# Kernel optimization log

Measured on AMD Instinct MI355X. Metric: run time of the kernel, lower is better.

Reference implementation:

```python
import jax, jax.numpy as jnp
import numpy as np

DIM = 1024
HEADS = 16
DIM_HEAD = 64
INNER = HEADS * DIM_HEAD
B, N = 2, 2048


def rope_encoding(seq_len, dim_head):
    inv_freq = 1.0 / (10000.0 ** (jnp.arange(0, dim_head, 2, dtype=jnp.float32) / dim_head))
    pos = jnp.arange(seq_len, dtype=jnp.float32)
    sinusoid = pos[:, None] * inv_freq[None, :]          # [n, d/2]
    return jnp.concatenate([jnp.sin(sinusoid), jnp.cos(sinusoid)], axis=-1)  # [n, d]


def setup_inputs() -> dict:
    key = jax.random.key(0)
    k1, k2, k3, k4 = jax.random.split(key, 4)
    feats = jax.random.normal(k1, (B, N, DIM), dtype=jnp.float32)
    mask = jnp.ones((B, N), dtype=bool)
    # params (torch Linear: y = x @ W.T + b; store as [in, out] for x @ W)
    W_qkv = jax.random.normal(k2, (DIM, 3 * INNER), dtype=jnp.float32) / np.sqrt(DIM)
    W_out = jax.random.normal(k3, (INNER, DIM), dtype=jnp.float32) / np.sqrt(INNER)
    b_out = jax.random.normal(k4, (DIM,), dtype=jnp.float32) * 0.01
    return {"feats": feats, "W_qkv": W_qkv, "W_out": W_out, "b_out": b_out, "mask": mask}


def reference(feats, W_qkv, W_out, b_out, mask):
    b, n, _ = feats.shape
    h, d = HEADS, DIM_HEAD
    scale = d ** -0.5

    qkv = feats @ W_qkv                                   # [b, n, 3*inner]
    q, k, v = jnp.split(qkv, 3, axis=-1)
    to_bhnd = lambda t: t.reshape(b, n, h, d).transpose(0, 2, 1, 3)
    q, k, v = to_bhnd(q), to_bhnd(k), to_bhnd(v)          # [b, h, n, d]

    rope = rope_encoding(n, d)                            # [n, d]
    q = q + rope
    k = k + rope

    m = mask[:, None, :, None]                            # [b, 1, n, 1]
    neg_max = -jnp.finfo(k.dtype).max
    k = jnp.where(m, k, neg_max)

    q = jax.nn.softmax(q, axis=-1)                        # over feature dim
    k = jax.nn.softmax(k, axis=-2)                        # over sequence dim
    q = q * scale
    v = jnp.where(m, v, 0.0)

    context = jnp.einsum('bhnd,bhne->bhde', k, v)         # [b, h, d, d]
    out = jnp.einsum('bhde,bhnd->bhne', context, q)       # [b, h, n, d]
    out = out.transpose(0, 2, 1, 3).reshape(b, n, h * d)  # [b, n, inner]
    out = out @ W_out + b_out                             # [b, n, dim]

    attn = jnp.einsum('bhnd,bhmd->bhnm', q, k) * scale    # [b, h, n, n]
    return out, attn
```

## Files before the change

kernel.cpp:

```cpp
#include <hip/hip_runtime.h>
#include <cstddef>


#define BB     2
#define SEQ    2048
#define DIMM   1024
#define NHEADS 16
#define DH     64
#define TRIPLE 3072
#define ROWS   (BB*SEQ)
#define SCALE  0.125f

typedef unsigned short u16;
typedef unsigned int   u32;
typedef short s16x8 __attribute__((ext_vector_type(8)));
typedef float f32x4 __attribute__((ext_vector_type(4)));
typedef float vf4   __attribute__((ext_vector_type(4)));

static constexpr size_t WS_QB    = 0;
static constexpr size_t WS_KB    = 8388608;
static constexpr size_t WS_DEN   = 16777216;
static constexpr size_t WS_CTX   = 16785408;
static constexpr size_t WS_ROPET = 17309696;
static constexpr size_t WS_AQPK  = 17833984;
static constexpr size_t WS_W2PK  = 34611200;

static constexpr size_t SC_QKV  = 0;
static constexpr size_t SC_APK  = 50331648;
static constexpr size_t SC_WQPK = 67108864;

__device__ __forceinline__ u16 f2bf(float x) {
    u32 u = __float_as_uint(x);
    return (u16)((u + 0x7fffu + ((u >> 16) & 1u)) >> 16);
}
__device__ __forceinline__ float bf2f(u16 h) {
    return __uint_as_float(((u32)h) << 16);
}
__device__ __forceinline__ void glds16(const char* g, char* l) {
    __builtin_amdgcn_global_load_lds(
        (const __attribute__((address_space(1))) void*)g,
        (__attribute__((address_space(3))) void*)l, 16, 0, 0);
}

__device__ __forceinline__ void conv_pack_item(const float* __restrict__ src,
                                               u16* __restrict__ dst, int t)
{
    int g  = t & 3;
    int kb = (t >> 2) & 31;
    int row = t >> 7;
    const float* s = src + (size_t)row * 1024 + kb * 32 + 4 * g;
    float4 xa = *(const float4*)s;
    float4 xb = *(const float4*)(s + 16);
    float xs[8] = {xa.x, xa.y, xa.z, xa.w, xb.x, xb.y, xb.z, xb.w};
    s16x8 hv, lv;
    #pragma unroll
    for (int e = 0; e < 8; ++e) {
        u16 h = f2bf(xs[e]);
        hv[e] = (short)h;
        lv[e] = (short)f2bf(xs[e] - bf2f(h));
    }
    size_t rowc = (size_t)row * 256 + kb * 8;
    int sw = row & 7;
    *(s16x8*)(dst + (rowc + (size_t)(g ^ sw)) * 8)       = hv;
    *(s16x8*)(dst + (rowc + (size_t)((4 | g) ^ sw)) * 8) = lv;
}

__global__ __launch_bounds__(256)
void prologue(float4* __restrict__ denctx, float4* __restrict__ ropeT,
              const float* __restrict__ feats, u16* __restrict__ A_pk,
              const float* __restrict__ Wqkv, u16* __restrict__ Wq_pk)
{
    __shared__ float fb[32][128];
    const int bid = blockIdx.x, tid = threadIdx.x;
    if (bid < 130) {
        denctx[bid * 256 + tid] = float4{0.f, 0.f, 0.f, 0.f};
        return;
    }
    if (bid < 258) {
        int t = (bid - 130) * 256 + tid;
        int pos = t >> 4, r16 = t & 15;
        double a0 = (double)pos * pow(10000.0, -(double)r16 / 32.0);
        double a1 = (double)pos * pow(10000.0, -(double)(r16 + 16) / 32.0);
        float4 v;
        v.x = (float)sin(a0); v.y = (float)sin(a1);
        v.z = (float)cos(a0); v.w = (float)cos(a1);
        ropeT[t] = v;
        return;
    }
    if (bid < 2306) {
        conv_pack_item(feats, A_pk, (bid - 258) * 256 + tid);
        return;
    }
    {
        int cb = bid - 2306;
        int n0 = (cb % 24) * 128, kb = cb / 24, k0 = kb * 32;
        #pragma unroll
        for (int q = 0; q < 4; ++q) {
            int cc = q * 256 + tid;
            int kr = cc >> 5, nc = (cc & 31) * 4;
            *(float4*)&fb[kr][nc] = *(const float4*)&Wqkv[(size_t)(k0 + kr) * TRIPLE + n0 + nc];
        }
        __syncthreads();
        #pragma unroll
        for (int it = 0; it < 2; ++it) {
            int item = it * 256 + tid;
            int g = (item >> 7) & 3, n = item & 127;
            s16x8 hv, lv;
            #pragma unroll
            for (int e = 0; e < 4; ++e) {
                float x0 = fb[4 * g + e][n];
                float x1 = fb[16 + 4 * g + e][n];
                u16 h0 = f2bf(x0), h1 = f2bf(x1);
                hv[e]     = (short)h0;
                hv[e + 4] = (short)h1;
                lv[e]     = (short)f2bf(x0 - bf2f(h0));
                lv[e + 4] = (short)f2bf(x1 - bf2f(h1));
            }
            int row = n0 + n;
            size_t rowc = (size_t)row * 256 + kb * 8;
            int sw = row & 7;
            *(s16x8*)(Wq_pk + (rowc + (size_t)(g ^ sw)) * 8)       = hv;
            *(s16x8*)(Wq_pk + (rowc + (size_t)((4 | g) ^ sw)) * 8) = lv;
        }
    }
}

__global__ __launch_bounds__(256, 3)
void gemm_qkv(const u16* __restrict__ Ap, const u16* __restrict__ Bp,
              float* __restrict__ C, const float* __restrict__ ropeT,
              float* __restrict__ den)
{
    __shared__ __align__(16) char smem[32768];
    const int tid = threadIdx.x;
    const int lane = tid & 63, wid = tid >> 6;
    const int wi = wid >> 1, wj = wid & 1;
    const int r16 = lane & 15, g = lane >> 4;

    const int bid = blockIdx.x;
    const int swz = (bid & 7) * 96 + (bid >> 3);
    const int bx = swz % 24, by = swz / 24;
    const int brow = by * 128, bcol = bx * 128;

    const int srow = wid * 32 + (lane >> 3);
    const int sch  = lane & 7;
    const char* gA = (const char*)Ap + ((size_t)(brow + srow) * 256 + sch) * 16;
    const char* gB = (const char*)Bp + ((size_t)(bcol + srow) * 256 + sch) * 16;
    char* la = smem + wid * 4096;
    char* lb = smem + 16384 + wid * 4096;

    f32x4 acc[4][4] = {};
    size_t koff = 0;
    for (int kb = 0; kb < 32; ++kb, koff += 128) {
        #pragma unroll
        for (int q = 0; q < 4; ++q) {
            glds16(gA + (size_t)q * (8 * 4096) + koff, la + q * 1024);
            glds16(gB + (size_t)q * (8 * 4096) + koff, lb + q * 1024);
        }
        __syncthreads();
        s16x8 ah[4], al[4], bh[4], bl[4];
        #pragma unroll
        for (int i = 0; i < 4; ++i) {
            int ra = wi * 64 + i * 16 + r16;
            const s16x8* Ar = (const s16x8*)(smem + (size_t)ra * 128);
            ah[i] = Ar[g ^ (ra & 7)];
            al[i] = Ar[(4 | g) ^ (ra & 7)];
            int rb = wj * 64 + i * 16 + r16;
            const s16x8* Br = (const s16x8*)(smem + 16384 + (size_t)rb * 128);
            bh[i] = Br[g ^ (rb & 7)];
            bl[i] = Br[(4 | g) ^ (rb & 7)];
        }
        #pragma unroll
        for (int i = 0; i < 4; ++i)
            #pragma unroll
            for (int j = 0; j < 4; ++j) {
                acc[i][j] = __builtin_amdgcn_mfma_f32_16x16x32_bf16(ah[i], bh[j], acc[i][j], 0, 0, 0);
                acc[i][j] = __builtin_amdgcn_mfma_f32_16x16x32_bf16(ah[i], bl[j], acc[i][j], 0, 0, 0);
                acc[i][j] = __builtin_amdgcn_mfma_f32_16x16x32_bf16(al[i], bh[j], acc[i][j], 0, 0, 0);
            }
        __syncthreads();
    }

    const int pos0 = brow & (SEQ - 1);
    const vf4* rT = (const vf4*)ropeT;
    if (bx < 8) {
        #pragma unroll
        for (int i = 0; i < 4; ++i)
            #pragma unroll
            for (int r = 0; r < 4; ++r) {
                int rloc = wi * 64 + i * 16 + g * 4 + r;
                vf4 rv = rT[(size_t)(pos0 + rloc) * 16 + r16];
                float v[4];
                #pragma unroll
                for (int j = 0; j < 4; ++j) v[j] = acc[i][j][r] + rv[j];
                float m = fmaxf(fmaxf(v[0], v[1]), fmaxf(v[2], v[3]));
                #pragma unroll
                for (int o = 1; o <= 8; o <<= 1) m = fmaxf(m, __shfl_xor(m, o));
                float e[4];
                float s = 0.f;
                #pragma unroll
                for (int j = 0; j < 4; ++j) { e[j] = expf(v[j] - m); s += e[j]; }
                #pragma unroll
                for (int o = 1; o <= 8; o <<= 1) s += __shfl_xor(s, o);
                float inv = SCALE / s;
                size_t rb = (size_t)(brow + rloc) * TRIPLE + bcol + wj * 64;
                #pragma unroll
                for (int j = 0; j < 4; ++j)
                    C[rb + j * 16 + r16] = e[j] * inv;
            }
    } else if (bx < 16) {
        float dsum[4] = {0.f, 0.f, 0.f, 0.f};
        #pragma unroll
        for (int i = 0; i < 4; ++i)
            #pragma unroll
            for (int r = 0; r < 4; ++r) {
                int rloc = wi * 64 + i * 16 + g * 4 + r;
                vf4 rv = rT[(size_t)(pos0 + rloc) * 16 + r16];
                size_t rb = (size_t)(brow + rloc) * TRIPLE + bcol + wj * 64;
                #pragma unroll
                for (int j = 0; j < 4; ++j) {
                    float e = expf(acc[i][j][r] + rv[j]);
                    C[rb + j * 16 + r16] = e;
                    dsum[j] += e;
                }
            }
        const int bD = (brow >> 11) * DIMM;
        #pragma unroll
        for (int j = 0; j < 4; ++j) {
            float s = dsum[j];
            s += __shfl_xor(s, 16);
            s += __shfl_xor(s, 32);
            if (g == 0)
                atomicAdd(&den[bD + (bcol - DIMM) + wj * 64 + j * 16 + r16], s);
        }
    } else {
        #pragma unroll
        for (int i = 0; i < 4; ++i) {
            int row = brow + wi * 64 + i * 16 + g * 4;
            #pragma unroll
            for (int j = 0; j < 4; ++j) {
                int col = bcol + wj * 64 + j * 16 + r16;
                #pragma unroll
                for (int r = 0; r < 4; ++r)
                    C[(size_t)(row + r) * TRIPLE + col] = acc[i][j][r];
            }
        }
    }
}

__global__ __launch_bounds__(256)
void packctx(const float* __restrict__ qkv, const float* __restrict__ den,
             u16* __restrict__ qb, u16* __restrict__ kb,
             u16* __restrict__ Aq_pk, float* __restrict__ ctx)
{
    __shared__ float kt[32][64];
    __shared__ float vt[32][64];
    if (blockIdx.x < 2048) {
        int t = blockIdx.x * 256 + threadIdx.x;
        int g  = t & 3;
        int db = (t >> 2) & 1;
        int h  = (t >> 3) & 15;
        int row = t >> 7;
        int b = row >> 11, n = row & (SEQ - 1);
        size_t dst = ((size_t)(b * NHEADS + h) * SEQ + n) * 64 + db * 32 + g * 8;
        const float* sq = qkv + (size_t)row * TRIPLE + h * DH + db * 32 + 4 * g;
        {
            float4 xa = *(const float4*)sq;
            float4 xb = *(const float4*)(sq + 16);
            float xs[8] = {xa.x, xa.y, xa.z, xa.w, xb.x, xb.y, xb.z, xb.w};
            s16x8 hv, lv;
            #pragma unroll
            for (int e = 0; e < 8; ++e) {
                u16 hh = f2bf(xs[e]);
                hv[e] = (short)hh;
                lv[e] = (short)f2bf(xs[e] - bf2f(hh));
            }
            *(s16x8*)(qb + dst) = hv;
            int sw = row & 7;
            size_t base = (size_t)row * 2048 + (size_t)(h * 2 + db) * 64;
            *(s16x8*)(Aq_pk + base + (size_t)((g ^ sw) * 8))       = hv;
            *(s16x8*)(Aq_pk + base + (size_t)((((4 | g) ^ sw)) * 8)) = lv;
        }
        {
            const float* sk = sq + DIMM;
            const float* dn = den + (size_t)b * DIMM + h * DH + db * 32 + 4 * g;
            float4 xa = *(const float4*)sk;
            float4 xb = *(const float4*)(sk + 16);
            float4 da = *(const float4*)dn;
            float4 dc = *(const float4*)(dn + 16);
            float xs[8] = {xa.x / da.x, xa.y / da.y, xa.z / da.z, xa.w / da.w,
                           xb.x / dc.x, xb.y / dc.y, xb.z / dc.z, xb.w / dc.w};
            s16x8 hv;
            #pragma unroll
            for (int e = 0; e < 8; ++e) hv[e] = (short)f2bf(xs[e]);
            *(s16x8*)(kb + dst) = hv;
        }
        return;
    }
    int cb = blockIdx.x - 2048;
    int chunk = cb & 7, h = (cb >> 3) & 15, b = cb >> 7;
    int row0 = b * SEQ + chunk * 256;
    int d  = threadIdx.x & 63;
    int eg = threadIdx.x >> 6;
    float acc[16] = {};
    for (int t = 0; t < 8; ++t) {
        #pragma unroll
        for (int q = 0; q < 2; ++q) {
            int lf = threadIdx.x * 2 + q;
            int nn = lf >> 4;
            int c4 = (lf & 15) * 4;
            size_t base = (size_t)(row0 + t * 32 + nn) * TRIPLE + DIMM + h * DH + c4;
            *(float4*)&kt[nn][c4] = *(const float4*)&qkv[base];
            *(float4*)&vt[nn][c4] = *(const float4*)&qkv[base + DIMM];
        }
        __syncthreads();
        #pragma unroll 8
        for (int nn = 0; nn < 32; ++nn) {
            float kv = kt[nn][d];
            #pragma unroll
            for (int j = 0; j < 16; ++j)
                acc[j] = fmaf(kv, vt[nn][eg * 16 + j], acc[j]);
        }
        __syncthreads();
    }
    float rden = 1.f / den[(size_t)b * DIMM + h * DH + d];
    size_t cbase = ((size_t)(b * NHEADS + h)) * (DH * DH) + d * DH + eg * 16;
    #pragma unroll
    for (int j = 0; j < 16; ++j) atomicAdd(&ctx[cbase + j], acc[j] * rden);
}

__global__ __launch_bounds__(256)
void W2k(const float* __restrict__ ctx, const float* __restrict__ Wout,
         u16* __restrict__ W2_pk)
{
    __shared__ float cl[64][64];
    const int bid = blockIdx.x, tid = threadIdx.x;
    const int ct = bid & 7, h = (bid >> 3) & 15, b = bid >> 7;
    const float* C = ctx + ((size_t)(b * NHEADS + h)) * (DH * DH);
    for (int i = tid; i < DH * DH; i += 256) cl[i >> 6][i & 63] = C[i];
    __syncthreads();
    const int c = ct * 128 + (tid & 127);
    const int dg = tid >> 7;
    float acc[32] = {};
    for (int e = 0; e < 64; ++e) {
        float wv = Wout[(size_t)(h * 64 + e) * DIMM + c];
        #pragma unroll
        for (int r = 0; r < 32; ++r)
            acc[r] = fmaf(cl[dg * 32 + r][e], wv, acc[r]);
    }
    s16x8 hv[4], lv[4];
    #pragma unroll
    for (int r = 0; r < 32; ++r) {
        int g2 = (r & 15) >> 2;
        int elem = (r & 3) + 4 * (r >> 4);
        u16 hh = f2bf(acc[r]);
        hv[g2][elem] = (short)hh;
        lv[g2][elem] = (short)f2bf(acc[r] - bf2f(hh));
    }
    const int sw = c & 7;
    u16* base = W2_pk + (size_t)b * 2097152 + (size_t)c * 2048 + (size_t)(h * 2 + dg) * 64;
    #pragma unroll
    for (int g2 = 0; g2 < 4; ++g2) {
        *(s16x8*)(base + ((g2 ^ sw) * 8))       = hv[g2];
        *(s16x8*)(base + (((4 | g2) ^ sw) * 8)) = lv[g2];
    }
}

__global__ __launch_bounds__(256, 2)
void epilogue2(const u16* __restrict__ Aq_pk, const u16* __restrict__ W2_pk,
               float* __restrict__ outp, const float* __restrict__ bias,
               const u16* __restrict__ qb, const u16* __restrict__ kb,
               float* __restrict__ attn)
{
    __shared__ __align__(16) char smem[65536];
    const int tid = threadIdx.x;
    const int lane = tid & 63, wid = tid >> 6;
    const int r16 = lane & 15, g = lane >> 4;
    const int bid = blockIdx.x;

    if (bid % 17 == 0) {
        const int gb = bid / 17;
        const int wi = wid >> 1, wj = wid & 1;
        const int swz = (gb & 7) * 64 + (gb >> 3);
        const int bx = swz >> 6, by = swz & 63;
        const int brow = by * 64, bcol = bx * 128;
        const int srA = wid * 16 + (lane >> 3);
        const int srB = wid * 32 + (lane >> 3);
        const int sch = lane & 7;
        const char* gA = (const char*)Aq_pk + ((size_t)(brow + srA) * 256 + sch) * 16;
        const char* gB = (const char*)(W2_pk + (size_t)(brow >> 11) * 2097152)
                         + ((size_t)(bcol + srB) * 256 + sch) * 16;

        auto STAGE = [&](int buf, int kb2) {
            size_t koff = (size_t)kb2 * 128;
            char* a = smem + buf * 24576 + wid * 2048;
            char* b = smem + buf * 24576 + 8192 + wid * 4096;
            #pragma unroll
            for (int q = 0; q < 2; ++q)
                glds16(gA + (size_t)q * (8 * 4096) + koff, a + q * 1024);
            #pragma unroll
            for (int q = 0; q < 4; ++q)
                glds16(gB + (size_t)q * (8 * 4096) + koff, b + q * 1024);
        };

        f32x4 acc[2][4] = {};
        STAGE(0, 0);
        __syncthreads();
        for (int kb2 = 0; kb2 < 32; ++kb2) {
            const int cur = kb2 & 1;
            if (kb2 < 31) STAGE(cur ^ 1, kb2 + 1);
            const char* Ab = smem + cur * 24576;
            const char* Bb = smem + cur * 24576 + 8192;
            s16x8 ah[2], al[2], bh[4], bl[4];
            #pragma unroll
            for (int i = 0; i < 2; ++i) {
                int ra = wi * 32 + i * 16 + r16;
                const s16x8* Ar = (const s16x8*)(Ab + (size_t)ra * 128);
                ah[i] = Ar[g ^ (ra & 7)];
                al[i] = Ar[(4 | g) ^ (ra & 7)];
            }
            #pragma unroll
            for (int j = 0; j < 4; ++j) {
                int rb = wj * 64 + j * 16 + r16;
                const s16x8* Br = (const s16x8*)(Bb + (size_t)rb * 128);
                bh[j] = Br[g ^ (rb & 7)];
                bl[j] = Br[(4 | g) ^ (rb & 7)];
            }
            #pragma unroll
            for (int i = 0; i < 2; ++i)
                #pragma unroll
                for (int j = 0; j < 4; ++j) {
                    acc[i][j] = __builtin_amdgcn_mfma_f32_16x16x32_bf16(ah[i], bh[j], acc[i][j], 0, 0, 0);
                    acc[i][j] = __builtin_amdgcn_mfma_f32_16x16x32_bf16(ah[i], bl[j], acc[i][j], 0, 0, 0);
                    acc[i][j] = __builtin_amdgcn_mfma_f32_16x16x32_bf16(al[i], bh[j], acc[i][j], 0, 0, 0);
                }
            __syncthreads();
        }
        #pragma unroll
        for (int i = 0; i < 2; ++i) {
            int row = brow + wi * 32 + i * 16 + g * 4;
            #pragma unroll
            for (int j = 0; j < 4; ++j) {
                int col = bcol + wj * 64 + j * 16 + r16;
                float bv = bias[col];
                #pragma unroll
                for (int r = 0; r < 4; ++r)
                    outp[(size_t)(row + r) * DIMM + col] = acc[i][j][r] + bv;
            }
        }
        return;
    }

    const int ab = bid - bid / 17 - 1;
    const int bh = ab >> 8;
    const int n0 = ((ab >> 4) & 15) * 128, m0 = (ab & 15) * 128;
    const int wi = wid >> 1, wj = wid & 1;
    float* ost = (float*)smem;
    const u16* qB = qb + (size_t)bh * (SEQ * 64);
    const u16* kB = kb + (size_t)bh * (SEQ * 64);
    f32x4 acc[4][4] = {};
    #pragma unroll
    for (int db = 0; db < 2; ++db) {
        s16x8 a[4], b[4];
        #pragma unroll
        for (int i = 0; i < 4; ++i) {
            a[i] = *(const s16x8*)(qB + (size_t)(n0 + wi * 64 + i * 16 + r16) * 64 + db * 32 + g * 8);
            b[i] = *(const s16x8*)(kB + (size_t)(m0 + wj * 64 + i * 16 + r16) * 64 + db * 32 + g * 8);
        }
        #pragma unroll
        for (int i = 0; i < 4; ++i)
            #pragma unroll
            for (int j = 0; j < 4; ++j)
                acc[i][j] = __builtin_amdgcn_mfma_f32_16x16x32_bf16(a[i], b[j], acc[i][j], 0, 0, 0);
    }
    #pragma unroll
    for (int i = 0; i < 4; ++i)
        #pragma unroll
        for (int j = 0; j < 4; ++j)
            #pragma unroll
            for (int r = 0; r < 4; ++r)
                ost[(wi * 64 + i * 16 + g * 4 + r) * 128 + wj * 64 + j * 16 + r16] =
                    acc[i][j][r] * SCALE;
    __syncthreads();
    size_t base = (size_t)bh * ((size_t)SEQ * SEQ) + (size_t)n0 * SEQ + m0;
    int rr = tid >> 5, c16 = tid & 31;
    #pragma unroll
    for (int it = 0; it < 16; ++it) {
        int row = rr * 16 + it;
        vf4 v = *(vf4*)&ost[row * 128 + c16 * 4];
        __builtin_nontemporal_store(v, (vf4*)&attn[base + (size_t)row * SEQ + c16 * 4]);
    }
}

extern "C" void kernel_launch(void* const* d_in, const int* in_sizes, int n_in,
                              void* d_out, int out_size, void* d_ws, size_t ws_size,
                              hipStream_t stream)
{
    const float* feats = (const float*)d_in[0];
    const float* Wqkv  = (const float*)d_in[1];
    const float* Wout  = (const float*)d_in[2];
    const float* bout  = (const float*)d_in[3];

    char*  wsb   = (char*)d_ws;
    u16*   qb    = (u16*)(wsb + WS_QB);
    u16*   kb    = (u16*)(wsb + WS_KB);
    float* den   = (float*)(wsb + WS_DEN);
    float* ctx   = (float*)(wsb + WS_CTX);
    float* ropeT = (float*)(wsb + WS_ROPET);
    u16*   Aq_pk = (u16*)(wsb + WS_AQPK);
    u16*   W2_pk = (u16*)(wsb + WS_W2PK);

    float* out  = (float*)d_out;
    float* attn = out + (size_t)ROWS * DIMM;
    char*  sc   = (char*)attn;
    float* qkv   = (float*)(sc + SC_QKV);
    u16*   A_pk  = (u16*)(sc + SC_APK);
    u16*   Wq_pk = (u16*)(sc + SC_WQPK);

    prologue<<<3074, 256, 0, stream>>>((float4*)den, (float4*)ropeT,
                                       feats, A_pk, Wqkv, Wq_pk);
    gemm_qkv<<<768, 256, 0, stream>>>(A_pk, Wq_pk, qkv, ropeT, den);
    packctx<<<2304, 256, 0, stream>>>(qkv, den, qb, kb, Aq_pk, ctx);
    W2k<<<256, 256, 0, stream>>>(ctx, Wout, W2_pk);
    epilogue2<<<8704, 256, 0, stream>>>(Aq_pk, W2_pk, out, bout, qb, kb, attn);
}
```

Before: 338.6 us.

## Fuse q bf16 packing into QKV GEMM epilogue and reorder epilogue block interleave

The QKV GEMM's q-softmax epilogue now writes the bf16 hi/lo split straight into qb and the swizzled Aq_pk layout, so the fp32 q values no longer round-trip through global memory. packctx shrinks to handling only k (four chunks per thread) plus the context reduction, launching fewer blocks. The epilogue kernel changes how it interleaves out-projection GEMM blocks with attention blocks, putting them all at the front (every third block). The trade-off is that the fused q stores are scattered 2-byte writes instead of 16-byte vector stores.

```diff
diff --git a/kernel.cpp b/kernel.cpp
--- a/kernel.cpp
+++ b/kernel.cpp
@@ -128,7 +128,8 @@
 __global__ __launch_bounds__(256, 3)
 void gemm_qkv(const u16* __restrict__ Ap, const u16* __restrict__ Bp,
               float* __restrict__ C, const float* __restrict__ ropeT,
-              float* __restrict__ den)
+              float* __restrict__ den, u16* __restrict__ qb,
+              u16* __restrict__ Aq_pk)
 {
     __shared__ __align__(16) char smem[32768];
     const int tid = threadIdx.x;
@@ -183,6 +184,7 @@
     const int pos0 = brow & (SEQ - 1);
     const vf4* rT = (const vf4*)ropeT;
     if (bx < 8) {
+        const int h = bx * 2 + wj;
         #pragma unroll
         for (int i = 0; i < 4; ++i)
             #pragma unroll
@@ -202,10 +204,24 @@
                 #pragma unroll
                 for (int o = 1; o <= 8; o <<= 1) s += __shfl_xor(s, o);
                 float inv = SCALE / s;
-                size_t rb = (size_t)(brow + rloc) * TRIPLE + bcol + wj * 64;
-                #pragma unroll
-                for (int j = 0; j < 4; ++j)
-                    C[rb + j * 16 + r16] = e[j] * inv;
+                int grow = brow + rloc;
+                int b = grow >> 11, n = grow & (SEQ - 1);
+                size_t qbbase = ((size_t)(b * NHEADS + h) * SEQ + n) * 64;
+                int sw = grow & 7;
+                size_t aqbase = (size_t)grow * 2048;
+                int g2 = r16 >> 2;
+                #pragma unroll
+                for (int j = 0; j < 4; ++j) {
+                    float qv = e[j] * inv;
+                    u16 hi = f2bf(qv);
+                    u16 lo = f2bf(qv - bf2f(hi));
+                    int db = j >> 1;
+                    int elem = (r16 & 3) + 4 * (j & 1);
+                    qb[qbbase + db * 32 + g2 * 8 + elem] = hi;
+                    size_t ab = aqbase + (size_t)(h * 2 + db) * 64;
+                    Aq_pk[ab + ((g2 ^ sw) * 8 + elem)]       = hi;
+                    Aq_pk[ab + (((4 | g2) ^ sw) * 8 + elem)] = lo;
+                }
             }
     } else if (bx < 16) {
         float dsum[4] = {0.f, 0.f, 0.f, 0.f};
@@ -249,54 +265,35 @@
 
 __global__ __launch_bounds__(256)
 void packctx(const float* __restrict__ qkv, const float* __restrict__ den,
-             u16* __restrict__ qb, u16* __restrict__ kb,
-             u16* __restrict__ Aq_pk, float* __restrict__ ctx)
+             u16* __restrict__ kb, float* __restrict__ ctx)
 {
     __shared__ float kt[32][64];
     __shared__ float vt[32][64];
-    if (blockIdx.x < 2048) {
+    if (blockIdx.x < 512) {
         int t = blockIdx.x * 256 + threadIdx.x;
-        int g  = t & 3;
-        int db = (t >> 2) & 1;
-        int h  = (t >> 3) & 15;
-        int row = t >> 7;
+        int db = t & 1;
+        int h  = (t >> 1) & 15;
+        int row = t >> 5;
         int b = row >> 11, n = row & (SEQ - 1);
-        size_t dst = ((size_t)(b * NHEADS + h) * SEQ + n) * 64 + db * 32 + g * 8;
-        const float* sq = qkv + (size_t)row * TRIPLE + h * DH + db * 32 + 4 * g;
-        {
-            float4 xa = *(const float4*)sq;
-            float4 xb = *(const float4*)(sq + 16);
-            float xs[8] = {xa.x, xa.y, xa.z, xa.w, xb.x, xb.y, xb.z, xb.w};
-            s16x8 hv, lv;
-            #pragma unroll
-            for (int e = 0; e < 8; ++e) {
-                u16 hh = f2bf(xs[e]);
-                hv[e] = (short)hh;
-                lv[e] = (short)f2bf(xs[e] - bf2f(hh));
-            }
-            *(s16x8*)(qb + dst) = hv;
-            int sw = row & 7;
-            size_t base = (size_t)row * 2048 + (size_t)(h * 2 + db) * 64;
-            *(s16x8*)(Aq_pk + base + (size_t)((g ^ sw) * 8))       = hv;
-            *(s16x8*)(Aq_pk + base + (size_t)((((4 | g) ^ sw)) * 8)) = lv;
-        }
-        {
-            const float* sk = sq + DIMM;
-            const float* dn = den + (size_t)b * DIMM + h * DH + db * 32 + 4 * g;
-            float4 xa = *(const float4*)sk;
-            float4 xb = *(const float4*)(sk + 16);
-            float4 da = *(const float4*)dn;
-            float4 dc = *(const float4*)(dn + 16);
+        size_t dst = ((size_t)(b * NHEADS + h) * SEQ + n) * 64 + db * 32;
+        const float* sk = qkv + (size_t)row * TRIPLE + DIMM + h * DH + db * 32;
+        const float* dn = den + (size_t)b * DIMM + h * DH + db * 32;
+        #pragma unroll
+        for (int g = 0; g < 4; ++g) {
+            float4 xa = *(const float4*)(sk + 4 * g);
+            float4 xb = *(const float4*)(sk + 16 + 4 * g);
+            float4 da = *(const float4*)(dn + 4 * g);
+            float4 dc = *(const float4*)(dn + 16 + 4 * g);
             float xs[8] = {xa.x / da.x, xa.y / da.y, xa.z / da.z, xa.w / da.w,
                            xb.x / dc.x, xb.y / dc.y, xb.z / dc.z, xb.w / dc.w};
             s16x8 hv;
             #pragma unroll
             for (int e = 0; e < 8; ++e) hv[e] = (short)f2bf(xs[e]);
-            *(s16x8*)(kb + dst) = hv;
+            *(s16x8*)(kb + dst + g * 8) = hv;
         }
         return;
     }
-    int cb = blockIdx.x - 2048;
+    int cb = blockIdx.x - 512;
     int chunk = cb & 7, h = (cb >> 3) & 15, b = cb >> 7;
     int row0 = b * SEQ + chunk * 256;
     int d  = threadIdx.x & 63;
@@ -377,8 +374,8 @@
     const int r16 = lane & 15, g = lane >> 4;
     const int bid = blockIdx.x;
 
-    if (bid % 17 == 0) {
-        const int gb = bid / 17;
+    if (bid < 1536 && bid % 3 == 0) {
+        const int gb = bid / 3;
         const int wi = wid >> 1, wj = wid & 1;
         const int swz = (gb & 7) * 64 + (gb >> 3);
         const int bx = swz >> 6, by = swz & 63;
@@ -450,7 +447,7 @@
         return;
     }
 
-    const int ab = bid - bid / 17 - 1;
+    const int ab = (bid < 1536) ? (bid - bid / 3 - 1) : (1024 + bid - 1536);
     const int bh = ab >> 8;
     const int n0 = ((ab >> 4) & 15) * 128, m0 = (ab & 15) * 128;
     const int wi = wid >> 1, wj = wid & 1;
@@ -518,8 +515,8 @@
 
     prologue<<<3074, 256, 0, stream>>>((float4*)den, (float4*)ropeT,
                                        feats, A_pk, Wqkv, Wq_pk);
-    gemm_qkv<<<768, 256, 0, stream>>>(A_pk, Wq_pk, qkv, ropeT, den);
-    packctx<<<2304, 256, 0, stream>>>(qkv, den, qb, kb, Aq_pk, ctx);
+    gemm_qkv<<<768, 256, 0, stream>>>(A_pk, Wq_pk, qkv, ropeT, den, qb, Aq_pk);
+    packctx<<<768, 256, 0, stream>>>(qkv, den, kb, ctx);
     W2k<<<256, 256, 0, stream>>>(ctx, Wout, W2_pk);
     epilogue2<<<8704, 256, 0, stream>>>(Aq_pk, W2_pk, out, bout, qb, kb, attn);
 }
```

After: 318.7 us, median of 2. -5.9%, faster.
